# Kernel optimization log

Measured on AMD Instinct MI355X. Metric: run time of the kernel, lower is better.

Reference implementation:

```python
import jax, jax.numpy as jnp
import numpy as np

PI = jnp.pi


def _spow(t, p):
    # t >= 0; safe t**p with value 0 (and zero grad) at t == 0
    tt = jnp.where(t > 0, t, 1.0)
    return jnp.where(t > 0, tt ** p, 0.0)


def _wavelets(t, f, fm, pm, em, fo, ph):
    # t: [L]; f: [S,1] -> returns [S, L] bank of wavelets (one per scale)
    sigma = jnp.maximum(fm / (2.0 * PI * f), 1e-6)        # [S,1]
    br = jnp.cos(2.0 * PI * f * t)                        # [S,L]
    bi = jnp.sin(2.0 * PI * f * t)
    # real_part: + pm0*br - c^2 (t/sig)^fo0 br pm1 + ... alternating, c = 2..7
    real = br * pm[0]
    sign = -1.0
    for j in range(6):
        c = j + 2.0
        real = real + sign * (_spow(t, fo[j]) * c / sigma ** fo[j] * c) * br * pm[j + 1]
        sign = -sign
    # imag_part: same pattern with fo6..fo11, pm8..pm13; j==9 term has the
    # anomalous parenthesization from the source: t**fo*5/(sigma**fo*5)
    imag = bi * pm[7]
    sign = -1.0
    for j in range(6, 12):
        c = j - 4.0
        if j == 9:
            term = (_spow(t, fo[j]) * 5.0 / (sigma ** fo[j] * 5.0)) * bi * pm[j + 2]
        else:
            term = (_spow(t, fo[j]) * c / sigma ** fo[j] * c) * bi * pm[j + 2]
        imag = imag + sign * term
        sign = -sign
    gauss = em[0] * jnp.exp(-t ** 2 / (2.0 * sigma ** 2))  # [S,L]
    rw = real * gauss
    iw = imag * gauss
    amp = rw + iw
    samp = amp / jnp.linalg.norm(amp, axis=-1, keepdims=True)
    phase = jnp.arctan2(iw, rw)
    w = (samp * jnp.sin(phase) * ph[0]) * (samp * jnp.cos(phase) * ph[1]) \
        * (samp * jnp.sinc(phase / PI) * ph[2])
    return w


def reference(x, scales, f_mod, poly_mod, exp_mod, frac_order, phase_mod, i):
    B, C = x.shape[0], x.shape[1]
    xf = x.reshape(B, C, -1)                              # [B,C,L]
    L = xf.shape[-1]
    S = scales.shape[0]
    t = jnp.arange(L, dtype=x.dtype)
    f = (1.0 / scales)[:, None]                           # [S,1]
    W = _wavelets(t, f, f_mod[i], poly_mod[i], exp_mod[i], frac_order[i],
                  phase_mod[i])                            # [S,L] kernels, K = L
    # torch F.conv1d(padding='same', groups=C*S) = cross-correlation with
    # left pad (K-1)//2. Computed exactly via zero-padded FFT linear conv.
    K = L
    Nfft = 2 * L                                          # >= L + K - 1, no aliasing
    Xf = jnp.fft.rfft(xf, n=Nfft, axis=-1)                # [B,C,F]
    Wf = jnp.fft.rfft(W[:, ::-1], n=Nfft, axis=-1)        # [S,F] (corr = conv w/ flip)
    y = jnp.fft.irfft(Xf[:, :, None, :] * Wf[None, None], n=Nfft, axis=-1)  # [B,C,S,2L]
    left = (K - 1) // 2
    off = K - 1 - left
    y = y[..., off:off + L]                               # [B,C,S,L]
    # torch channel layout: out[:, j] = corr(x[:, j % C], wavelet[j % S])
    j = jnp.arange(C * S)
    return y[:, j % C, j % S, :]                          # [B, C*S, L]


def setup_inputs() -> dict:
    key = jax.random.key(0)
    ks = jax.random.split(key, 6)
    B, C, H, Wd = 16, 16, 64, 64
    S, NSTEPS = 16, 10
    x = jax.random.normal(ks[0], (B, C, H, Wd), dtype=jnp.float32)
    scales = jnp.linspace(1.0, 32.0, S, dtype=jnp.float32)
    f_mod = 1.0 + 0.02 * jax.random.normal(ks[1], (NSTEPS,), dtype=jnp.float32)
    poly_mod = 1.0 + 0.02 * jax.random.normal(ks[2], (NSTEPS, 14), dtype=jnp.float32)
    exp_mod = 1.0 + 0.02 * jax.random.normal(ks[3], (NSTEPS, 1), dtype=jnp.float32)
    frac_order = 1.0 + 0.02 * jax.random.normal(ks[4], (NSTEPS, 12), dtype=jnp.float32)
    phase_mod = 1.0 + 0.02 * jax.random.normal(ks[5], (NSTEPS, 3), dtype=jnp.float32)
    return {"x": x, "scales": scales, "f_mod": f_mod, "poly_mod": poly_mod,
            "exp_mod": exp_mod, "frac_order": frac_order,
            "phase_mod": phase_mod, "i": 3}
```

## Files before the change

### kernel.cpp

```cpp
#include <hip/hip_runtime.h>
#include <math.h>

#define QMAX 128
#define ZCUT 1920
#define HALF 1088
#define XWIN 1216
#define XS_SZ 1280

typedef float vfloat4 __attribute__((ext_vector_type(4)));

__global__ void wavelet_build(const float* __restrict__ scales,
                              const float* __restrict__ f_mod,
                              const float* __restrict__ poly_mod,
                              const float* __restrict__ exp_mod,
                              const float* __restrict__ frac_order,
                              const float* __restrict__ phase_mod,
                              const int* __restrict__ istep,
                              float* __restrict__ Wout) {
    const int k = blockIdx.x;
    const int t = threadIdx.x;
    const int i = istep[0];
    const float PI2 = 6.28318530717958647692f;

    const float f = 1.0f / scales[k];
    const float fm = f_mod[i];
    const float* pm = poly_mod + i * 14;
    const float em0 = exp_mod[i];
    const float* fo = frac_order + i * 12;
    const float* ph = phase_mod + i * 3;

    const float sigma = fmaxf(fm / (PI2 * f), 1e-6f);
    const float tf = (float)t;
    const float arg = PI2 * f * tf;
    const float br = cosf(arg);
    const float bi = sinf(arg);

    float rp = pm[0];
    float sign = -1.0f;
    for (int j = 0; j < 6; ++j) {
        float c = (float)(j + 2);
        float sp = (tf > 0.0f) ? powf(tf, fo[j]) : 0.0f;
        rp += sign * (sp * c / powf(sigma, fo[j]) * c * pm[j + 1]);
        sign = -sign;
    }
    float ipoly = pm[7];
    sign = -1.0f;
    for (int j = 6; j < 12; ++j) {
        float sp = (tf > 0.0f) ? powf(tf, fo[j]) : 0.0f;
        float term;
        if (j == 9) {
            term = sp * 5.0f / (powf(sigma, fo[j]) * 5.0f) * pm[j + 2];
        } else {
            float c = (float)(j - 4);
            term = sp * c / powf(sigma, fo[j]) * c * pm[j + 2];
        }
        ipoly += sign * term;
        sign = -sign;
    }

    const float gauss = em0 * expf(-tf * tf / (2.0f * sigma * sigma));
    const float rw = br * rp * gauss;
    const float iw = bi * ipoly * gauss;
    const float amp = rw + iw;

    float sq = amp * amp;
    #pragma unroll
    for (int off = 32; off > 0; off >>= 1) sq += __shfl_xor(sq, off, 64);
    __shared__ float wsum[2];
    if ((t & 63) == 0) wsum[t >> 6] = sq;
    __syncthreads();
    const float norm = sqrtf(wsum[0] + wsum[1]);

    const float samp = amp / norm;
    const float phase = atan2f(iw, rw);
    const float sphi = sinf(phase);
    const float cphi = cosf(phase);
    const float snc = (phase != 0.0f) ? (sphi / phase) : 1.0f;
    Wout[k * QMAX + t] = (samp * sphi * ph[0]) * (samp * cphi * ph[1]) * (samp * snc * ph[2]);
}

__global__ __launch_bounds__(256) void conv_half(const float* __restrict__ x,
                                                 const float* __restrict__ W,
                                                 float* __restrict__ ws) {
    __shared__ __attribute__((aligned(16))) float xs[XS_SZ];
    __shared__ __attribute__((aligned(16))) float Wl[QMAX];

    const int blk = blockIdx.x;
    const int bk = blk >> 1;
    const int h = blk & 1;
    const int k = bk & 15;
    const int tid = threadIdx.x;
    const int Ph = ZCUT + h * HALF;

    if (tid < QMAX) Wl[tid] = W[k * QMAX + tid];

    const float* xrow = x + (size_t)bk * 4096;
    const int x0 = Ph - 2047;
    for (int li = tid; li < XS_SZ; li += 256) {
        int g = x0 + li;
        xs[li] = (g >= 0 && li < XWIN) ? xrow[g] : 0.0f;
    }
    __syncthreads();

    float* wrow = ws + (size_t)bk * 4096;
    #pragma unroll
    for (int e = 0; e < 2; ++e) {
        const int fi = tid + e * 256;
        if (e == 1 && fi >= HALF / 4) break;
        const int p = Ph + 4 * fi;
        const int base = 4 * fi;
        float acc[4] = {0.0f, 0.0f, 0.0f, 0.0f};
        float4 xcur = *(const float4*)&xs[base];
        for (int q = 0; q < QMAX; q += 4) {
            float4 w4 = *(const float4*)&Wl[q];
            float4 xnxt = *(const float4*)&xs[base + q + 4];
            float win[8] = {xcur.x, xcur.y, xcur.z, xcur.w,
                            xnxt.x, xnxt.y, xnxt.z, xnxt.w};
            float wv[4] = {w4.x, w4.y, w4.z, w4.w};
            #pragma unroll
            for (int j = 0; j < 4; ++j) {
                #pragma unroll
                for (int r = 0; r < 4; ++r) {
                    acc[r] = fmaf(win[r + j], wv[j], acc[r]);
                }
            }
            xcur = xnxt;
        }
        *(float4*)&wrow[p] = make_float4(acc[0], acc[1], acc[2], acc[3]);
    }
}

__global__ __launch_bounds__(256) void replicate_rows(const float* __restrict__ ws,
                                                      float* __restrict__ out) {
    const int g = blockIdx.x;
    const int m0 = g * 8;
    const int b = m0 >> 8;
    const int tid = threadIdx.x;
    const vfloat4 zero = {0.0f, 0.0f, 0.0f, 0.0f};

    #pragma unroll
    for (int r = 0; r < 8; ++r) {
        const int m = m0 + r;
        const int k = m & 15;
        const float* __restrict__ src = ws + ((size_t)b * 16 + k) * 4096;
        float* __restrict__ dst = out + (size_t)m * 4096;
        #pragma unroll
        for (int v = 0; v < 4; ++v) {
            const int e = 4 * (tid + 256 * v);
            vfloat4 val = (e >= ZCUT) ? *(const vfloat4*)&src[e] : zero;
            __builtin_nontemporal_store(val, (vfloat4*)&dst[e]);
        }
    }
}

extern "C" void kernel_launch(void* const* d_in, const int* in_sizes, int n_in,
                              void* d_out, int out_size, void* d_ws, size_t ws_size,
                              hipStream_t stream) {
    const float* x          = (const float*)d_in[0];
    const float* scales     = (const float*)d_in[1];
    const float* f_mod      = (const float*)d_in[2];
    const float* poly_mod   = (const float*)d_in[3];
    const float* exp_mod    = (const float*)d_in[4];
    const float* frac_order = (const float*)d_in[5];
    const float* phase_mod  = (const float*)d_in[6];
    const int*   istep      = (const int*)d_in[7];
    float* out = (float*)d_out;
    float* wsd = (float*)d_ws;
    float* Wtab = wsd;
    float* rows = wsd + 4096;

    wavelet_build<<<dim3(16), dim3(QMAX), 0, stream>>>(
        scales, f_mod, poly_mod, exp_mod, frac_order, phase_mod, istep, Wtab);

    conv_half<<<dim3(512), dim3(256), 0, stream>>>(x, Wtab, rows);

    replicate_rows<<<dim3(512), dim3(256), 0, stream>>>(rows, out);
}
```

Before: 41.46 us.

## Fuse wavelet construction into conv kernel and use grid-stride replicate

Removes the separate wavelet_build launch: each conv block now computes the 128-tap wavelet for its scale in-kernel, overlapping that work with the x window load into shared memory. This cuts one kernel launch and the global round trip for the wavelet table, but every one of the 512 blocks recomputes the wavelet, with its many powf calls. The replicate kernel becomes a grid-stride loop over 2048 blocks using ordinary stores instead of nontemporal stores, which changes the write pattern for the large output.

```diff
diff --git a/kernel.cpp b/kernel.cpp
--- a/kernel.cpp
+++ b/kernel.cpp
@@ -9,81 +9,18 @@
 
 typedef float vfloat4 __attribute__((ext_vector_type(4)));
 
-__global__ void wavelet_build(const float* __restrict__ scales,
-                              const float* __restrict__ f_mod,
-                              const float* __restrict__ poly_mod,
-                              const float* __restrict__ exp_mod,
-                              const float* __restrict__ frac_order,
-                              const float* __restrict__ phase_mod,
-                              const int* __restrict__ istep,
-                              float* __restrict__ Wout) {
-    const int k = blockIdx.x;
-    const int t = threadIdx.x;
-    const int i = istep[0];
-    const float PI2 = 6.28318530717958647692f;
-
-    const float f = 1.0f / scales[k];
-    const float fm = f_mod[i];
-    const float* pm = poly_mod + i * 14;
-    const float em0 = exp_mod[i];
-    const float* fo = frac_order + i * 12;
-    const float* ph = phase_mod + i * 3;
-
-    const float sigma = fmaxf(fm / (PI2 * f), 1e-6f);
-    const float tf = (float)t;
-    const float arg = PI2 * f * tf;
-    const float br = cosf(arg);
-    const float bi = sinf(arg);
-
-    float rp = pm[0];
-    float sign = -1.0f;
-    for (int j = 0; j < 6; ++j) {
-        float c = (float)(j + 2);
-        float sp = (tf > 0.0f) ? powf(tf, fo[j]) : 0.0f;
-        rp += sign * (sp * c / powf(sigma, fo[j]) * c * pm[j + 1]);
-        sign = -sign;
-    }
-    float ipoly = pm[7];
-    sign = -1.0f;
-    for (int j = 6; j < 12; ++j) {
-        float sp = (tf > 0.0f) ? powf(tf, fo[j]) : 0.0f;
-        float term;
-        if (j == 9) {
-            term = sp * 5.0f / (powf(sigma, fo[j]) * 5.0f) * pm[j + 2];
-        } else {
-            float c = (float)(j - 4);
-            term = sp * c / powf(sigma, fo[j]) * c * pm[j + 2];
-        }
-        ipoly += sign * term;
-        sign = -sign;
-    }
-
-    const float gauss = em0 * expf(-tf * tf / (2.0f * sigma * sigma));
-    const float rw = br * rp * gauss;
-    const float iw = bi * ipoly * gauss;
-    const float amp = rw + iw;
-
-    float sq = amp * amp;
-    #pragma unroll
-    for (int off = 32; off > 0; off >>= 1) sq += __shfl_xor(sq, off, 64);
-    __shared__ float wsum[2];
-    if ((t & 63) == 0) wsum[t >> 6] = sq;
-    __syncthreads();
-    const float norm = sqrtf(wsum[0] + wsum[1]);
-
-    const float samp = amp / norm;
-    const float phase = atan2f(iw, rw);
-    const float sphi = sinf(phase);
-    const float cphi = cosf(phase);
-    const float snc = (phase != 0.0f) ? (sphi / phase) : 1.0f;
-    Wout[k * QMAX + t] = (samp * sphi * ph[0]) * (samp * cphi * ph[1]) * (samp * snc * ph[2]);
-}
-
 __global__ __launch_bounds__(256) void conv_half(const float* __restrict__ x,
-                                                 const float* __restrict__ W,
+                                                 const float* __restrict__ scales,
+                                                 const float* __restrict__ f_mod,
+                                                 const float* __restrict__ poly_mod,
+                                                 const float* __restrict__ exp_mod,
+                                                 const float* __restrict__ frac_order,
+                                                 const float* __restrict__ phase_mod,
+                                                 const int* __restrict__ istep,
                                                  float* __restrict__ ws) {
     __shared__ __attribute__((aligned(16))) float xs[XS_SZ];
     __shared__ __attribute__((aligned(16))) float Wl[QMAX];
+    __shared__ float wsum[2];
 
     const int blk = blockIdx.x;
     const int bk = blk >> 1;
@@ -92,13 +29,74 @@
     const int tid = threadIdx.x;
     const int Ph = ZCUT + h * HALF;
 
-    if (tid < QMAX) Wl[tid] = W[k * QMAX + tid];
-
     const float* xrow = x + (size_t)bk * 4096;
     const int x0 = Ph - 2047;
     for (int li = tid; li < XS_SZ; li += 256) {
         int g = x0 + li;
         xs[li] = (g >= 0 && li < XWIN) ? xrow[g] : 0.0f;
+    }
+
+    float amp = 0.0f, rw = 0.0f, iw = 0.0f;
+    if (tid < QMAX) {
+        const int i = istep[0];
+        const float PI2 = 6.28318530717958647692f;
+        const float f = 1.0f / scales[k];
+        const float fm = f_mod[i];
+        const float* pm = poly_mod + i * 14;
+        const float em0 = exp_mod[i];
+        const float* fo = frac_order + i * 12;
+
+        const float sigma = fmaxf(fm / (PI2 * f), 1e-6f);
+        const float tf = (float)tid;
+        const float arg = PI2 * f * tf;
+        const float br = cosf(arg);
+        const float bi = sinf(arg);
+
+        float rp = pm[0];
+        float sign = -1.0f;
+        for (int j = 0; j < 6; ++j) {
+            float c = (float)(j + 2);
+            float sp = (tf > 0.0f) ? powf(tf, fo[j]) : 0.0f;
+            rp += sign * (sp * c / powf(sigma, fo[j]) * c * pm[j + 1]);
+            sign = -sign;
+        }
+        float ipoly = pm[7];
+        sign = -1.0f;
+        for (int j = 6; j < 12; ++j) {
+            float sp = (tf > 0.0f) ? powf(tf, fo[j]) : 0.0f;
+            float term;
+            if (j == 9) {
+                term = sp * 5.0f / (powf(sigma, fo[j]) * 5.0f) * pm[j + 2];
+            } else {
+                float c = (float)(j - 4);
+                term = sp * c / powf(sigma, fo[j]) * c * pm[j + 2];
+            }
+            ipoly += sign * term;
+            sign = -sign;
+        }
+
+        const float gauss = em0 * expf(-tf * tf / (2.0f * sigma * sigma));
+        rw = br * rp * gauss;
+        iw = bi * ipoly * gauss;
+        amp = rw + iw;
+
+        float sq = amp * amp;
+        #pragma unroll
+        for (int off = 32; off > 0; off >>= 1) sq += __shfl_xor(sq, off, 64);
+        if ((tid & 63) == 0) wsum[tid >> 6] = sq;
+    }
+    __syncthreads();
+
+    if (tid < QMAX) {
+        const int i = istep[0];
+        const float* ph = phase_mod + i * 3;
+        const float norm = sqrtf(wsum[0] + wsum[1]);
+        const float samp = amp / norm;
+        const float phase = atan2f(iw, rw);
+        const float sphi = sinf(phase);
+        const float cphi = cosf(phase);
+        const float snc = (phase != 0.0f) ? (sphi / phase) : 1.0f;
+        Wl[tid] = (samp * sphi * ph[0]) * (samp * cphi * ph[1]) * (samp * snc * ph[2]);
     }
     __syncthreads();
 
@@ -130,26 +128,21 @@
     }
 }
 
-__global__ __launch_bounds__(256) void replicate_rows(const float* __restrict__ ws,
-                                                      float* __restrict__ out) {
-    const int g = blockIdx.x;
-    const int m0 = g * 8;
-    const int b = m0 >> 8;
-    const int tid = threadIdx.x;
+__global__ __launch_bounds__(256) void replicate_gs(const float* __restrict__ ws,
+                                                    float* __restrict__ out) {
+    const int NF4 = 4096 * 1024;
+    const int stride = gridDim.x * blockDim.x;
     const vfloat4 zero = {0.0f, 0.0f, 0.0f, 0.0f};
-
-    #pragma unroll
-    for (int r = 0; r < 8; ++r) {
-        const int m = m0 + r;
+    for (int idx = blockIdx.x * blockDim.x + threadIdx.x; idx < NF4; idx += stride) {
+        const int m = idx >> 10;
+        const int p = (idx & 1023) * 4;
+        const int b = m >> 8;
         const int k = m & 15;
-        const float* __restrict__ src = ws + ((size_t)b * 16 + k) * 4096;
-        float* __restrict__ dst = out + (size_t)m * 4096;
-        #pragma unroll
-        for (int v = 0; v < 4; ++v) {
-            const int e = 4 * (tid + 256 * v);
-            vfloat4 val = (e >= ZCUT) ? *(const vfloat4*)&src[e] : zero;
-            __builtin_nontemporal_store(val, (vfloat4*)&dst[e]);
+        vfloat4 val = zero;
+        if (p >= ZCUT) {
+            val = *(const vfloat4*)&ws[(((size_t)b * 16 + k) << 12) + p];
         }
+        *(vfloat4*)&out[(size_t)idx * 4] = val;
     }
 }
 
@@ -165,14 +158,10 @@
     const float* phase_mod  = (const float*)d_in[6];
     const int*   istep      = (const int*)d_in[7];
     float* out = (float*)d_out;
-    float* wsd = (float*)d_ws;
-    float* Wtab = wsd;
-    float* rows = wsd + 4096;
+    float* rows = (float*)d_ws;
 
-    wavelet_build<<<dim3(16), dim3(QMAX), 0, stream>>>(
-        scales, f_mod, poly_mod, exp_mod, frac_order, phase_mod, istep, Wtab);
+    conv_half<<<dim3(512), dim3(256), 0, stream>>>(
+        x, scales, f_mod, poly_mod, exp_mod, frac_order, phase_mod, istep, rows);
 
-    conv_half<<<dim3(512), dim3(256), 0, stream>>>(x, Wtab, rows);
-
-    replicate_rows<<<dim3(512), dim3(256), 0, stream>>>(rows, out);
+    replicate_gs<<<dim3(2048), dim3(256), 0, stream>>>(rows, out);
 }
```

New measurement: 41.16 us. No clear change (-0.7%).
